# Kernel tuning notes

Measured on AMD Instinct MI355X. Metric: run time of the kernel, lower is better.

Reference implementation:

```python
import jax, jax.numpy as jnp
import numpy as np

B, GS, IN, HID = 256, 32, 512, 1024
HW = GS * GS

def setup_inputs() -> dict:
    key = jax.random.key(0)
    ks = jax.random.split(key, 18)
    s = 0.02
    return {
        "grid": jax.random.normal(ks[0], (B, 1, GS, GS), jnp.float32),
        "conv1_w": jax.random.normal(ks[1], (8, 1, 3, 3), jnp.float32) * s,
        "conv1_b": jax.random.normal(ks[2], (8,), jnp.float32) * s,
        "conv2_w": jax.random.normal(ks[3], (16, 8, 3, 3), jnp.float32) * s,
        "conv2_b": jax.random.normal(ks[4], (16,), jnp.float32) * s,
        "lin_w": jax.random.normal(ks[5], (IN, HW * 16), jnp.float32) * s,
        "lin_b": jax.random.normal(ks[6], (IN,), jnp.float32) * s,
        "gru_wih": jax.random.normal(ks[7], (3 * HID, IN + HW + 1), jnp.float32) * s,
        "gru_whh": jax.random.normal(ks[8], (3 * HID, HID), jnp.float32) * s,
        "gru_bih": jax.random.normal(ks[9], (3 * HID,), jnp.float32) * s,
        "gru_bhh": jax.random.normal(ks[10], (3 * HID,), jnp.float32) * s,
        "write_w": jax.random.normal(ks[11], (HW, HID), jnp.float32) * s,
        "write_b": jax.random.normal(ks[12], (HW,), jnp.float32) * s,
        "inc_w": jax.random.normal(ks[13], (1, HID), jnp.float32) * s,
        "inc_b": jax.random.normal(ks[14], (1,), jnp.float32) * s,
        "term_w": jax.random.normal(ks[15], (1, HID), jnp.float32) * s,
        "term_b": jax.random.normal(ks[16], (1,), jnp.float32) * s,
        "max_steps": 100,
    }

def _conv(x, w, b):
    y = jax.lax.conv_general_dilated(x, w, (1, 1), "SAME",
                                     dimension_numbers=("NCHW", "OIHW", "NCHW"))
    return y + b[None, :, None, None]

def _gru_cell(x, h, wih, whh, bih, bhh):
    gi = x @ wih.T + bih            # (B, 3H)
    gh = h @ whh.T + bhh
    ir, iz, inn = jnp.split(gi, 3, axis=1)
    hr, hz, hn = jnp.split(gh, 3, axis=1)
    r = jax.nn.sigmoid(ir + hr)
    z = jax.nn.sigmoid(iz + hz)
    n = jnp.tanh(inn + r * hn)
    return (1.0 - z) * n + z * h

def reference(grid, conv1_w, conv1_b, conv2_w, conv2_b, lin_w, lin_b,
              gru_wih, gru_whh, gru_bih, gru_bhh,
              write_w, write_b, inc_w, inc_b, term_w, term_b, max_steps):
    bsz = grid.shape[0]
    feat = jax.nn.relu(_conv(grid, conv1_w, conv1_b))
    feat = jax.nn.relu(_conv(feat, conv2_w, conv2_b))
    feat = feat.reshape(bsz, -1) @ lin_w.T + lin_b     # (B, IN), torch Flatten is channel-major

    def step(carry, _):
        h, mask, count, done = carry
        x = jnp.concatenate([feat, mask, count], axis=1)
        h2 = _gru_cell(x, h, gru_wih, gru_whh, gru_bih, gru_bhh)
        write = jax.nn.sigmoid(h2 @ write_w.T + write_b)
        inc = jax.nn.sigmoid(h2 @ inc_w.T + inc_b)
        term = jax.nn.sigmoid(h2 @ term_w.T + term_b)
        upd = jnp.logical_not(done)
        h_n = jnp.where(upd, h2, h)
        mask_n = jnp.where(upd, mask + write, mask)
        count_n = jnp.where(upd, count + inc, count)
        done_n = jnp.logical_or(done, jnp.all(term > 0.5))
        return (h_n, mask_n, count_n, done_n), None

    init = (jnp.zeros((bsz, HID), grid.dtype),
            jnp.zeros((bsz, HW), grid.dtype),
            jnp.zeros((bsz, 1), grid.dtype),
            jnp.array(False))
    (h, mask, count, done), _ = jax.lax.scan(step, init, None, length=max_steps)
    return count, mask
```

## Files before the change

kernel.cpp:

```cpp
#include <hip/hip_runtime.h>
#include <hip/hip_bf16.h>
#include <hip/hip_cooperative_groups.h>

namespace cg = cooperative_groups;

#define DEVI static __device__ __forceinline__

typedef __attribute__((ext_vector_type(8))) short s8v;
typedef __attribute__((ext_vector_type(4))) float f32x4;
typedef unsigned short us_t;
typedef unsigned int u32;

constexpr int NT_ = 256;
constexpr int B_ = 256, HW_ = 1024, IN_ = 512, HID_ = 1024, H3_ = 3072;
constexpr int XD_ = 1537;
constexpr int FLAT_ = 16384;

constexpr int OFF_WIHFBF = 0;
constexpr int OFF_WIHM2  = 393216;
constexpr int OFF_WIHC   = 5111808;
constexpr int OFF_CNTD   = 5114880;
constexpr int OFF_FLAGS  = 5115136;
constexpr int OFF_FEATBF = 5115264;
constexpr int OFF_GI     = 5180800;
constexpr int OFF_GH     = 5967232;
constexpr int OFF_H0     = 6753664;
constexpr int OFF_H1     = 7015808;
constexpr int OFF_WSIG   = 7277952;
constexpr int OFF_HHI    = 7540096;
constexpr int OFF_WSIG2  = 7671168;
constexpr int OFF_C2BF   = 7933312;
constexpr int OFF_PART = OFF_GI;
constexpr int OFF_PW   = OFF_C2BF;
constexpr int OFF_PA2  = 14224768;

struct Params {
  const float* grid;
  const float* c1w; const float* c1b;
  const float* c2w; const float* c2b;
  const float* linw; const float* linb;
  const float* wih; const float* whh;
  const float* bih; const float* bhh;
  const float* ww;  const float* wb;
  const float* incw; const float* incb;
  const float* termw; const float* termb;
  const int* max_steps;
  float* out;
  float* ws;
};

DEVI float sigm(float x) { return 1.f / (1.f + __expf(-x)); }
DEVI float tanh_(float x) { return 1.f - 2.f / (__expf(2.f * x) + 1.f); }
DEVI float2 ld2(const float* p) { return *(const float2*)p; }
DEVI void ld4(float* d, const float* p) {
  float4 v = *(const float4*)p; d[0] = v.x; d[1] = v.y; d[2] = v.z; d[3] = v.w;
}
DEVI us_t f2bf(float x) {
  union { float f; u32 u; } v; v.f = x;
  u32 r = v.u + 0x7FFFu + ((v.u >> 16) & 1u);
  return (us_t)(r >> 16);
}
DEVI float bf2f(us_t h) {
  union { u32 u; float f; } v; v.u = ((u32)h) << 16; return v.f;
}
DEVI u32 pack2(float a, float b) { return (u32)f2bf(a) | ((u32)f2bf(b) << 16); }
DEVI u32 pack2c(float a, float b) {
  __hip_bfloat162 h = __float22bfloat162_rn(make_float2(a, b));
  union { __hip_bfloat162 h; u32 u; } v; v.h = h; return v.u;
}

DEVI s8v ld8w(const us_t* p) { return *(const s8v*)p; }
DEVI s8v ld8w(const float* p) {
  float4 v0 = *(const float4*)p;
  float4 v1 = *(const float4*)(p + 4);
  union { u32 u[4]; s8v s; } r;
  r.u[0] = pack2c(v0.x, v0.y); r.u[1] = pack2c(v0.z, v0.w);
  r.u[2] = pack2c(v1.x, v1.y); r.u[3] = pack2c(v1.z, v1.w);
  return r.s;
}

__global__ __launch_bounds__(NT_) void conv_kernel(Params p) {
  __shared__ float s_in[34 * 34];
  __shared__ float s_c1[8 * 34 * 34];
  const int b = blockIdx.x;
  const int tid = threadIdx.x;
  for (int i = tid; i < 34 * 34; i += NT_) s_in[i] = 0.f;
  for (int i = tid; i < 8 * 34 * 34; i += NT_) s_c1[i] = 0.f;
  __syncthreads();
  for (int i = tid; i < 1024; i += NT_) {
    int y = i >> 5, x = i & 31;
    s_in[(y + 1) * 34 + (x + 1)] = p.grid[b * 1024 + i];
  }
  __syncthreads();
  const int pos0 = tid * 4;
  const int y = pos0 >> 5, x0 = pos0 & 31;
  {
    float win[3][6];
    #pragma unroll
    for (int dy = 0; dy < 3; ++dy)
      #pragma unroll
      for (int c = 0; c < 6; ++c) win[dy][c] = s_in[(y + dy) * 34 + x0 + c];
    float acc[8][4];
    #pragma unroll
    for (int oc = 0; oc < 8; ++oc)
      #pragma unroll
      for (int i = 0; i < 4; ++i) acc[oc][i] = p.c1b[oc];
    #pragma unroll
    for (int oc = 0; oc < 8; ++oc)
      #pragma unroll
      for (int dy = 0; dy < 3; ++dy)
        #pragma unroll
        for (int dx = 0; dx < 3; ++dx) {
          float w = p.c1w[oc * 9 + dy * 3 + dx];
          #pragma unroll
          for (int i = 0; i < 4; ++i)
            acc[oc][i] = fmaf(w, win[dy][i + dx], acc[oc][i]);
        }
    #pragma unroll
    for (int oc = 0; oc < 8; ++oc)
      #pragma unroll
      for (int i = 0; i < 4; ++i)
        s_c1[oc * 1156 + (y + 1) * 34 + (x0 + i + 1)] = fmaxf(acc[oc][i], 0.f);
  }
  __syncthreads();
  {
    float acc[16][4];
    #pragma unroll
    for (int oc = 0; oc < 16; ++oc)
      #pragma unroll
      for (int i = 0; i < 4; ++i) acc[oc][i] = p.c2b[oc];
    for (int ic = 0; ic < 8; ++ic) {
      float win[3][6];
      #pragma unroll
      for (int dy = 0; dy < 3; ++dy)
        #pragma unroll
        for (int c = 0; c < 6; ++c)
          win[dy][c] = s_c1[ic * 1156 + (y + dy) * 34 + x0 + c];
      #pragma unroll
      for (int oc = 0; oc < 16; ++oc)
        #pragma unroll
        for (int dy = 0; dy < 3; ++dy)
          #pragma unroll
          for (int dx = 0; dx < 3; ++dx) {
            float w = p.c2w[oc * 72 + ic * 9 + dy * 3 + dx];
            #pragma unroll
            for (int i = 0; i < 4; ++i)
              acc[oc][i] = fmaf(w, win[dy][i + dx], acc[oc][i]);
          }
    }
    us_t* dst = (us_t*)(p.ws + OFF_C2BF) + b * FLAT_;
    #pragma unroll
    for (int oc = 0; oc < 16; ++oc) {
      u32 lo = pack2(fmaxf(acc[oc][0], 0.f), fmaxf(acc[oc][1], 0.f));
      u32 hi = pack2(fmaxf(acc[oc][2], 0.f), fmaxf(acc[oc][3], 0.f));
      *(uint2*)(dst + oc * 1024 + pos0) = make_uint2(lo, hi);
    }
  }
}

template <typename TA, typename TB>
DEVI void mfma_blockT(const TA* __restrict__ Ag, int lda,
                      const TB* __restrict__ Bg, int ldb, int nc,
                      us_t* __restrict__ sA, us_t* __restrict__ sB,
                      float* __restrict__ dst, int ldd) {
  const int tid = threadIdx.x;
  const int ar = tid >> 3, au = tid & 7;
  const int sw = au ^ (ar & 7);
  const int abase = (ar * 8 + sw) * 8;
  const TA* a0p = Ag + (size_t)ar * lda + au * 8;
  const TA* a1p = Ag + (size_t)(ar + 32) * lda + au * 8;
  const TB* b0p = Bg + (size_t)ar * ldb + au * 8;
  const TB* b1p = b0p + (size_t)32 * ldb;
  const TB* b2p = b0p + (size_t)64 * ldb;
  const TB* b3p = b0p + (size_t)96 * ldb;
  f32x4 acc[4][2];
  #pragma unroll
  for (int f = 0; f < 4; ++f) { acc[f][0] = (f32x4)0.f; acc[f][1] = (f32x4)0.f; }
  s8v ra0 = ld8w(a0p);
  s8v ra1 = ld8w(a1p);
  s8v rb0 = ld8w(b0p);
  s8v rb1 = ld8w(b1p);
  s8v rb2 = ld8w(b2p);
  s8v rb3 = ld8w(b3p);
  const int w = tid >> 6;
  const int lane = tid & 63;
  const int l15 = lane & 15, l4 = lane >> 4;
  const int rsw = l15 & 7;
  int c = 0;
  for (;;) {
    __syncthreads();
    *(s8v*)(sA + abase) = ra0;
    *(s8v*)(sA + abase + 2048) = ra1;
    *(s8v*)(sB + abase) = rb0;
    *(s8v*)(sB + abase + 2048) = rb1;
    *(s8v*)(sB + abase + 4096) = rb2;
    *(s8v*)(sB + abase + 6144) = rb3;
    ++c;
    if (c < nc) {
      const int ko = c * 64;
      ra0 = ld8w(a0p + ko);
      ra1 = ld8w(a1p + ko);
      rb0 = ld8w(b0p + ko);
      rb1 = ld8w(b1p + ko);
      rb2 = ld8w(b2p + ko);
      rb3 = ld8w(b3p + ko);
    }
    __syncthreads();
    #pragma unroll
    for (int kk = 0; kk < 2; ++kk) {
      const int uoff = ((kk * 4 + l4) ^ rsw) * 8;
      s8v bA = *(const s8v*)(sB + (w * 32 + l15) * 64 + uoff);
      s8v bB = *(const s8v*)(sB + (w * 32 + 16 + l15) * 64 + uoff);
      #pragma unroll
      for (int f = 0; f < 4; ++f) {
        s8v a = *(const s8v*)(sA + (f * 16 + l15) * 64 + uoff);
        acc[f][0] = __builtin_amdgcn_mfma_f32_16x16x32_bf16(a, bA, acc[f][0], 0, 0, 0);
        acc[f][1] = __builtin_amdgcn_mfma_f32_16x16x32_bf16(a, bB, acc[f][1], 0, 0, 0);
      }
    }
    if (c >= nc) break;
  }
  #pragma unroll
  for (int f = 0; f < 4; ++f)
    #pragma unroll
    for (int g = 0; g < 2; ++g) {
      float* dp = dst + (size_t)(f * 16 + l4 * 4) * ldd + w * 32 + g * 16 + l15;
      #pragma unroll
      for (int j = 0; j < 4; ++j) dp[(size_t)j * ldd] = acc[f][g][j];
    }
}

__global__ __launch_bounds__(NT_) void lin_mfma(Params p) {
  __shared__ us_t sm[12288];
  const int j = (blockIdx.x >> 3) + (blockIdx.x & 7) * 32;
  const int mt = j & 3, nt = (j >> 2) & 3, ks = j >> 4;
  const us_t* A = (us_t*)(p.ws + OFF_C2BF) + (size_t)mt * 64 * FLAT_ + ks * 1024;
  const float* B = p.linw + (size_t)nt * 128 * FLAT_ + ks * 1024;
  float* dst = p.ws + OFF_PART + ks * (B_ * IN_) + mt * 64 * IN_ + nt * 128;
  mfma_blockT(A, FLAT_, B, FLAT_, 16, sm, sm + 4096, dst, IN_);
}

__global__ __launch_bounds__(NT_) void prepred_kernel(Params p) {
  const int tid = threadIdx.x;
  if (blockIdx.x < 512) {
    const int gt = blockIdx.x * NT_ + tid;
    const int o = gt & (IN_ - 1);
    const float* part = p.ws + OFF_PART;
    float s = p.linb[o];
    #pragma unroll
    for (int ks = 0; ks < 16; ++ks) s += part[ks * (B_ * IN_) + gt];
    ((us_t*)(p.ws + OFF_FEATBF))[gt] = f2bf(s);
  } else {
    const int gt = (blockIdx.x - 512) * NT_ + tid;
    const int gs = 1024 * NT_;
    us_t* wihf = (us_t*)(p.ws + OFF_WIHFBF);
    us_t* wihm2 = (us_t*)(p.ws + OFF_WIHM2);
    float* wihc = p.ws + OFF_WIHC;
    int* flags = (int*)(p.ws + OFF_FLAGS);
    for (int i = gt; i < H3_ * XD_; i += gs) {
      const int n = i / XD_, k = i - n * XD_;
      const float v = p.wih[i];
      if (k < 512) {
        wihf[n * 512 + k] = f2bf(v);
      } else if (k < 1536) {
        const int kk = k - 512;
        const us_t hi = f2bf(v);
        wihm2[n * 2048 + kk] = hi;
        wihm2[n * 2048 + 1024 + kk] = f2bf(v - bf2f(hi));
      } else {
        wihc[n] = v;
      }
    }
    if (gt < 128) flags[gt] = 1;
  }
}

__global__ __launch_bounds__(NT_) void a1_mfma(Params p) {
  __shared__ us_t sm[12288];
  const int b = blockIdx.x;
  const int mt = b / 24, nt = b - mt * 24;
  const us_t* A = (us_t*)(p.ws + OFF_FEATBF) + (size_t)mt * 64 * IN_;
  const us_t* B = (us_t*)(p.ws + OFF_WIHFBF) + (size_t)nt * 128 * IN_;
  float* dst = p.ws + OFF_GI + (size_t)mt * 64 * H3_ + nt * 128;
  mfma_blockT(A, IN_, B, IN_, 8, sm, sm + 4096, dst, H3_);
}

__global__ __launch_bounds__(NT_) void stepA_mfma(Params p, int step) {
  if (((volatile int*)(p.ws + OFF_FLAGS))[step - 1]) return;
  __shared__ us_t sm[12288];
  const int b = blockIdx.x;
  if (b < 576) {
    const int term = b / 192;
    const int r = b - term * 192;
    const int ks = r / 96;
    const int t = r - ks * 96;
    const int mt = t / 24, nt = t - mt * 24;
    const us_t* A = (us_t*)(p.ws + OFF_WSIG2) + (size_t)mt * 64 * 2048 +
                    (term == 1 ? 1024 : 0) + ks * 512;
    const us_t* B = (us_t*)(p.ws + OFF_WIHM2) + (size_t)nt * 128 * 2048 +
                    (term == 2 ? 1024 : 0) + ks * 512;
    float* dst = p.ws + OFF_PA2 + (size_t)(term * 2 + ks) * 786432 +
                 (size_t)mt * 64 * H3_ + nt * 128;
    mfma_blockT(A, 2048, B, 2048, 8, sm, sm + 4096, dst, H3_);
  } else {
    const int r = b - 576;
    const int ks = r / 96;
    const int t = r - ks * 96;
    const int mt = t / 24, nt = t - mt * 24;
    const us_t* A = (us_t*)(p.ws + OFF_HHI) + (size_t)mt * 64 * HID_ + ks * 512;
    const float* B = p.whh + (size_t)nt * 128 * HID_ + ks * 512;
    float* dst = p.ws + OFF_PA2 + (size_t)(6 + ks) * 786432 +
                 (size_t)mt * 64 * H3_ + nt * 128;
    mfma_blockT(A, HID_, B, HID_, 8, sm, sm + 4096, dst, H3_);
  }
}

__global__ __launch_bounds__(NT_) void stepG_kernel(Params p, int step) {
  int* flags = (int*)(p.ws + OFF_FLAGS);
  if (step > 0 && ((volatile int*)flags)[step - 1]) return;
  __shared__ float sred[8];
  const int row = blockIdx.x;
  const int tid = threadIdx.x;
  const size_t base = (size_t)row * H3_;
  float* const gi = p.ws + OFF_GI + base;
  const float* const pA = p.ws + OFF_PA2;
  const float* const wihc = p.ws + OFF_WIHC;
  const float* hold = p.ws + ((step & 1) ? OFF_H1 : OFF_H0) + (size_t)row * HID_;
  float* hnew = p.ws + ((step & 1) ? OFF_H0 : OFF_H1) + (size_t)row * HID_;
  us_t* hhi = (us_t*)(p.ws + OFF_HHI) + (size_t)row * HID_;
  const float cd = (step > 0) ? (p.ws + OFF_CNTD)[row] : 0.f;
  float incd = 0.f, termd = 0.f;
  #pragma unroll
  for (int q = 0; q < 4; ++q) {
    const int c = tid + q * NT_;
    float gr_ = gi[c], gz_ = gi[1024 + c], gn_ = gi[2048 + c];
    float hr_ = 0.f, hz_ = 0.f, hn_ = 0.f, hv = 0.f;
    if (step > 0) {
      #pragma unroll
      for (int t6 = 0; t6 < 6; ++t6) {
        const float* pp = pA + (size_t)t6 * 786432 + base;
        gr_ += pp[c]; gz_ += pp[1024 + c]; gn_ += pp[2048 + c];
      }
      gr_ += cd * wihc[c];
      gz_ += cd * wihc[1024 + c];
      gn_ += cd * wihc[2048 + c];
      const float* q6 = pA + (size_t)6 * 786432 + base;
      const float* q7 = pA + (size_t)7 * 786432 + base;
      hr_ = q6[c] + q7[c];
      hz_ = q6[1024 + c] + q7[1024 + c];
      hn_ = q6[2048 + c] + q7[2048 + c];
      gi[c] = gr_; gi[1024 + c] = gz_; gi[2048 + c] = gn_;
      hv = hold[c];
    }
    float rr = sigm(gr_ + p.bih[c] + hr_ + p.bhh[c]);
    float zz = sigm(gz_ + p.bih[1024 + c] + hz_ + p.bhh[1024 + c]);
    float nn = tanh_(gn_ + p.bih[2048 + c] + rr * (hn_ + p.bhh[2048 + c]));
    float h2 = (1.f - zz) * nn + zz * hv;
    hnew[c] = h2;
    hhi[c] = f2bf(h2);
    incd = fmaf(h2, p.incw[c], incd);
    termd = fmaf(h2, p.termw[c], termd);
  }
  #pragma unroll
  for (int off = 32; off > 0; off >>= 1) {
    incd += __shfl_down(incd, off);
    termd += __shfl_down(termd, off);
  }
  if ((tid & 63) == 0) { sred[tid >> 6] = incd; sred[4 + (tid >> 6)] = termd; }
  __syncthreads();
  if (tid == 0) {
    float it = sred[0] + sred[1] + sred[2] + sred[3];
    float tt = sred[4] + sred[5] + sred[6] + sred[7];
    float cdn = sigm(it + p.incb[0]);
    (p.ws + OFF_CNTD)[row] = cdn;
    if (step == 0) p.out[row] = cdn;
    else p.out[row] += cdn;
    if (tt + p.termb[0] <= 0.f) atomicAnd(&flags[step], 0);
  }
}

__global__ __launch_bounds__(NT_) void stepW_mfma(Params p, int step) {
  if (step > 0 && ((volatile int*)(p.ws + OFF_FLAGS))[step - 1]) return;
  __shared__ us_t sm[12288];
  const int b = blockIdx.x;
  const int ks = b & 7, t = b >> 3;
  const int mt = t >> 3, nt = t & 7;
  const us_t* A = (us_t*)(p.ws + OFF_HHI) + (size_t)mt * 64 * HID_ + ks * 128;
  const float* B = p.ww + (size_t)nt * 128 * HID_ + ks * 128;
  float* dst = p.ws + OFF_PW + ks * (B_ * HW_) + (size_t)mt * 64 * HW_ + nt * 128;
  mfma_blockT(A, HID_, B, HID_, 2, sm, sm + 4096, dst, HW_);
}

__global__ __launch_bounds__(NT_) void stepWepi_kernel(Params p, int step) {
  if (step > 0 && ((volatile int*)(p.ws + OFF_FLAGS))[step - 1]) return;
  const int i = (blockIdx.x * NT_ + threadIdx.x) * 4;
  const int m = i >> 10, n = i & 1023;
  const float* pW = p.ws + OFF_PW;
  float4 s = *(const float4*)(p.wb + n);
  #pragma unroll
  for (int ks = 0; ks < 8; ++ks) {
    float4 v = *(const float4*)(pW + ks * (B_ * HW_) + i);
    s.x += v.x; s.y += v.y; s.z += v.z; s.w += v.w;
  }
  float4 sv = {sigm(s.x), sigm(s.y), sigm(s.z), sigm(s.w)};
  float* op = p.out + B_ + i;
  if (step == 0) {
    *(float4*)op = sv;
  } else {
    float4 ov = *(float4*)op;
    ov.x += sv.x; ov.y += sv.y; ov.z += sv.z; ov.w += sv.w;
    *(float4*)op = ov;
  }
  *(float4*)(p.ws + OFF_WSIG + i) = sv;
  us_t* w2 = (us_t*)(p.ws + OFF_WSIG2) + (size_t)m * 2048 + n;
  us_t h0 = f2bf(sv.x), h1 = f2bf(sv.y), h2b = f2bf(sv.z), h3 = f2bf(sv.w);
  *(uint2*)w2 = make_uint2((u32)h0 | ((u32)h1 << 16), (u32)h2b | ((u32)h3 << 16));
  *(uint2*)(w2 + 1024) = make_uint2(
      pack2(sv.x - bf2f(h0), sv.y - bf2f(h1)),
      pack2(sv.z - bf2f(h2b), sv.w - bf2f(h3)));
}

DEVI void b_job(const Params& p, float* sh2, float* swb,
                const float* gi, const float* gh, const float* hold,
                float* hnew, float* wsig, float* cntd, int* dflag, int job) {
  const int tid = threadIdx.x;
  const int mt = job >> 3, nt = job & 7;
  const int r0 = mt * 8, c0 = nt * 128;
  const int gr = tid >> 5;
  const int gk = (tid & 31) * 2;
  const int wr = tid & 7;
  const int wc = (tid >> 3) * 4;
  const int row = r0 + gr;
  const float* giR = gi + row * H3_;
  const float* ghR = gh + row * H3_;
  const float* hR = hold + row * HID_;
  float* hW = hnew + row * HID_;
  float acc[4] = {0.f, 0.f, 0.f, 0.f};
  float incd = 0.f, termd = 0.f;
  const bool wh = (nt == 0);
  for (int kc = 0; kc < HID_; kc += 64) {
    float2 gxr = ld2(giR + kc + gk);
    float2 gxz = ld2(giR + 1024 + kc + gk);
    float2 gxn = ld2(giR + 2048 + kc + gk);
    float2 ghr = ld2(ghR + kc + gk);
    float2 ghz = ld2(ghR + 1024 + kc + gk);
    float2 ghn = ld2(ghR + 2048 + kc + gk);
    float2 hol = ld2(hR + kc + gk);
    float2 bri = ld2(p.bih + kc + gk);
    float2 brh = ld2(p.bhh + kc + gk);
    float2 bzi = ld2(p.bih + 1024 + kc + gk);
    float2 bzh = ld2(p.bhh + 1024 + kc + gk);
    float2 bni = ld2(p.bih + 2048 + kc + gk);
    float2 bnh = ld2(p.bhh + 2048 + kc + gk);
    float2 iw = ld2(p.incw + kc + gk);
    float2 tw = ld2(p.termw + kc + gk);
    float h2[2];
    {
      float rr = sigm(gxr.x + bri.x + ghr.x + brh.x);
      float zz = sigm(gxz.x + bzi.x + ghz.x + bzh.x);
      float nn = tanh_(gxn.x + bni.x + rr * (ghn.x + bnh.x));
      h2[0] = (1.f - zz) * nn + zz * hol.x;
      rr = sigm(gxr.y + bri.y + ghr.y + brh.y);
      zz = sigm(gxz.y + bzi.y + ghz.y + bzh.y);
      nn = tanh_(gxn.y + bni.y + rr * (ghn.y + bnh.y));
      h2[1] = (1.f - zz) * nn + zz * hol.y;
    }
    incd = fmaf(h2[0], iw.x, fmaf(h2[1], iw.y, incd));
    termd = fmaf(h2[0], tw.x, fmaf(h2[1], tw.y, termd));
    float4 wreg[8];
    #pragma unroll
    for (int it = 0; it < 8; ++it) {
      int id = tid + it * 256;
      int c = id >> 4, k4 = (id & 15) * 4;
      wreg[it] = *(const float4*)(p.ww + (c0 + c) * HID_ + kc + k4);
    }
    __syncthreads();
    sh2[gr * 68 + gk] = h2[0];
    sh2[gr * 68 + gk + 1] = h2[1];
    #pragma unroll
    for (int it = 0; it < 8; ++it) {
      int id = tid + it * 256;
      int c = id >> 4, k4 = (id & 15) * 4;
      swb[(k4 + 0) * 132 + c] = wreg[it].x;
      swb[(k4 + 1) * 132 + c] = wreg[it].y;
      swb[(k4 + 2) * 132 + c] = wreg[it].z;
      swb[(k4 + 3) * 132 + c] = wreg[it].w;
    }
    if (wh) {
      *(float2*)(hW + kc + gk) = make_float2(h2[0], h2[1]);
      *(u32*)((us_t*)(p.ws + OFF_HHI) + row * HID_ + kc + gk) = pack2(h2[0], h2[1]);
    }
    __syncthreads();
    #pragma unroll 8
    for (int kk = 0; kk < 64; ++kk) {
      float a = sh2[wr * 68 + kk];
      float4 b = *(const float4*)(swb + kk * 132 + wc);
      acc[0] = fmaf(a, b.x, acc[0]);
      acc[1] = fmaf(a, b.y, acc[1]);
      acc[2] = fmaf(a, b.z, acc[2]);
      acc[3] = fmaf(a, b.w, acc[3]);
    }
  }
  if (wh) {
    #pragma unroll
    for (int off = 16; off > 0; off >>= 1) {
      incd += __shfl_down(incd, off, 32);
      termd += __shfl_down(termd, off, 32);
    }
    if ((tid & 31) == 0) {
      float cd = sigm(incd + p.incb[0]);
      cntd[row] = cd;
      p.out[row] += cd;
      if (termd + p.termb[0] <= 0.f) atomicAnd(dflag, 0);
    }
  }
  {
    const int m = r0 + wr;
    float4 wb4 = *(const float4*)(p.wb + c0 + wc);
    float4 sv = {sigm(acc[0] + wb4.x), sigm(acc[1] + wb4.y),
                 sigm(acc[2] + wb4.z), sigm(acc[3] + wb4.w)};
    float* op = p.out + B_ + m * HW_ + c0 + wc;
    float4 ov = *(float4*)op;
    ov.x += sv.x; ov.y += sv.y; ov.z += sv.z; ov.w += sv.w;
    *(float4*)op = ov;
    *(float4*)(wsig + m * HID_ + c0 + wc) = sv;
    us_t* w2 = (us_t*)(p.ws + OFF_WSIG2) + m * 2048 + c0 + wc;
    us_t h0 = f2bf(sv.x), h1 = f2bf(sv.y), h2b = f2bf(sv.z), h3 = f2bf(sv.w);
    *(uint2*)w2 = make_uint2((u32)h0 | ((u32)h1 << 16), (u32)h2b | ((u32)h3 << 16));
    *(uint2*)(w2 + 1024) = make_uint2(
        pack2(sv.x - bf2f(h0), sv.y - bf2f(h1)),
        pack2(sv.z - bf2f(h2b), sv.w - bf2f(h3)));
  }
}

template <bool SB>
DEVI void gemm_db64(const float* __restrict__ A, int lda,
                    const float* __restrict__ Bw, int ldb, int K,
                    float* __restrict__ As, float* __restrict__ Bs,
                    float (&acc)[4][4]) {
  constexpr int P = 68;
  const int tid = threadIdx.x;
  const int tx = tid & 15, ty = tid >> 4;
  const int lr = tid >> 2, lk = (tid & 3) << 2;
  #pragma unroll
  for (int i = 0; i < 4; ++i)
    #pragma unroll
    for (int j = 0; j < 4; ++j) acc[i][j] = 0.f;
  auto ldb4 = [&](int k0) {
    float4 v;
    if constexpr (SB) {
      const float* q = Bw + (size_t)lr * ldb + k0 + lk;
      v.x = q[0]; v.y = q[1]; v.z = q[2]; v.w = q[3];
    } else {
      v = *(const float4*)(Bw + (size_t)lr * ldb + k0 + lk);
    }
    return v;
  };
  float4 va = *(const float4*)(A + lr * lda + lk);
  float4 vb = ldb4(0);
  As[(lk + 0) * P + lr] = va.x; As[(lk + 1) * P + lr] = va.y;
  As[(lk + 2) * P + lr] = va.z; As[(lk + 3) * P + lr] = va.w;
  Bs[(lk + 0) * P + lr] = vb.x; Bs[(lk + 1) * P + lr] = vb.y;
  Bs[(lk + 2) * P + lr] = vb.z; Bs[(lk + 3) * P + lr] = vb.w;
  __syncthreads();
  int cur = 0;
  for (int k0 = 16; k0 < K; k0 += 16) {
    va = *(const float4*)(A + lr * lda + k0 + lk);
    vb = ldb4(k0);
    const float* as = As + cur * (16 * P);
    const float* bs = Bs + cur * (16 * P);
    #pragma unroll
    for (int kk = 0; kk < 16; ++kk) {
      float a[4], b[4];
      ld4(a, as + kk * P + ty * 4);
      ld4(b, bs + kk * P + tx * 4);
      #pragma unroll
      for (int i = 0; i < 4; ++i)
        #pragma unroll
        for (int j = 0; j < 4; ++j) acc[i][j] = fmaf(a[i], b[j], acc[i][j]);
    }
    __syncthreads();
    float* asw = As + (cur ^ 1) * (16 * P);
    float* bsw = Bs + (cur ^ 1) * (16 * P);
    asw[(lk + 0) * P + lr] = va.x; asw[(lk + 1) * P + lr] = va.y;
    asw[(lk + 2) * P + lr] = va.z; asw[(lk + 3) * P + lr] = va.w;
    bsw[(lk + 0) * P + lr] = vb.x; bsw[(lk + 1) * P + lr] = vb.y;
    bsw[(lk + 2) * P + lr] = vb.z; bsw[(lk + 3) * P + lr] = vb.w;
    __syncthreads();
    cur ^= 1;
  }
  const float* as = As + cur * (16 * P);
  const float* bs = Bs + cur * (16 * P);
  #pragma unroll
  for (int kk = 0; kk < 16; ++kk) {
    float a[4], b[4];
    ld4(a, as + kk * P + ty * 4);
    ld4(b, bs + kk * P + tx * 4);
    #pragma unroll
    for (int i = 0; i < 4; ++i)
      #pragma unroll
      for (int j = 0; j < 4; ++j) acc[i][j] = fmaf(a[i], b[j], acc[i][j]);
  }
}

__global__ __launch_bounds__(NT_, 2) void tail_kernel(Params p, int start) {
  int* flags = (int*)(p.ws + OFF_FLAGS);
  if (((volatile int*)flags)[start - 1]) return;
  cg::grid_group gg = cg::this_grid();
  __shared__ __align__(16) float smem[8992];
  float* As = smem;
  float* Bs = smem + 2176;
  float* sh2 = smem;
  float* swb = smem + 544;
  float* const ws = p.ws;
  float* const gi = ws + OFF_GI;
  float* const gh = ws + OFF_GH;
  float* const wsig = ws + OFF_WSIG;
  float* const cntd = ws + OFF_CNTD;
  const float* const wihc = ws + OFF_WIHC;
  const int tid = threadIdx.x;
  const int bid = blockIdx.x;
  const int nb = gridDim.x;
  const int tx = tid & 15, ty = tid >> 4;
  const int msteps = p.max_steps[0];

  for (int step = start; step < msteps; ++step) {
    float* hcur = ws + ((step & 1) ? OFF_H1 : OFF_H0);
    float* hnxt = ws + ((step & 1) ? OFF_H0 : OFF_H1);
    for (int job = bid; job < 384; job += nb) {
      float acc[4][4];
      if (job < 192) {
        const int mt = job / 48, nt = job - mt * 48;
        gemm_db64<true>(wsig + mt * 64 * HID_, HID_,
                        p.wih + (size_t)nt * 64 * XD_ + 512, XD_, HID_, As, Bs, acc);
        #pragma unroll
        for (int i = 0; i < 4; ++i) {
          const int m = mt * 64 + ty * 4 + i;
          const float cd = cntd[m];
          float4 wc4 = *(const float4*)(wihc + nt * 64 + tx * 4);
          float* gp = gi + m * H3_ + nt * 64 + tx * 4;
          float4 g = *(float4*)gp;
          g.x += acc[i][0] + cd * wc4.x;
          g.y += acc[i][1] + cd * wc4.y;
          g.z += acc[i][2] + cd * wc4.z;
          g.w += acc[i][3] + cd * wc4.w;
          *(float4*)gp = g;
        }
      } else {
        const int j = job - 192;
        const int mt = j / 48, nt = j - mt * 48;
        gemm_db64<false>(hcur + mt * 64 * HID_, HID_,
                         p.whh + (size_t)nt * 64 * HID_, HID_, HID_, As, Bs, acc);
        #pragma unroll
        for (int i = 0; i < 4; ++i) {
          float4 v = {acc[i][0], acc[i][1], acc[i][2], acc[i][3]};
          *(float4*)(gh + (mt * 64 + ty * 4 + i) * H3_ + nt * 64 + tx * 4) = v;
        }
      }
      __syncthreads();
    }
    gg.sync();
    for (int job = bid; job < 256; job += nb)
      b_job(p, sh2, swb, gi, gh, hcur, hnxt, wsig, cntd, &flags[step], job);
    gg.sync();
    if (((volatile int*)flags)[step]) break;
  }
}

extern "C" void kernel_launch(void* const* d_in, const int* in_sizes, int n_in,
                              void* d_out, int out_size, void* d_ws, size_t ws_size,
                              hipStream_t stream) {
  (void)in_sizes; (void)n_in; (void)out_size; (void)ws_size;
  Params prm;
  prm.grid = (const float*)d_in[0];
  prm.c1w  = (const float*)d_in[1];
  prm.c1b  = (const float*)d_in[2];
  prm.c2w  = (const float*)d_in[3];
  prm.c2b  = (const float*)d_in[4];
  prm.linw = (const float*)d_in[5];
  prm.linb = (const float*)d_in[6];
  prm.wih  = (const float*)d_in[7];
  prm.whh  = (const float*)d_in[8];
  prm.bih  = (const float*)d_in[9];
  prm.bhh  = (const float*)d_in[10];
  prm.ww   = (const float*)d_in[11];
  prm.wb   = (const float*)d_in[12];
  prm.incw = (const float*)d_in[13];
  prm.incb = (const float*)d_in[14];
  prm.termw = (const float*)d_in[15];
  prm.termb = (const float*)d_in[16];
  prm.max_steps = (const int*)d_in[17];
  prm.out = (float*)d_out;
  prm.ws = (float*)d_ws;

  hipLaunchKernelGGL(conv_kernel, dim3(B_), dim3(NT_), 0, stream, prm);
  hipLaunchKernelGGL(lin_mfma, dim3(256), dim3(NT_), 0, stream, prm);
  hipLaunchKernelGGL(prepred_kernel, dim3(1536), dim3(NT_), 0, stream, prm);
  hipLaunchKernelGGL(a1_mfma, dim3(96), dim3(NT_), 0, stream, prm);

  constexpr int U = 2;
  hipLaunchKernelGGL(stepG_kernel, dim3(B_), dim3(NT_), 0, stream, prm, 0);
  hipLaunchKernelGGL(stepW_mfma, dim3(256), dim3(NT_), 0, stream, prm, 0);
  hipLaunchKernelGGL(stepWepi_kernel, dim3(256), dim3(NT_), 0, stream, prm, 0);
  for (int t = 1; t < U; ++t) {
    hipLaunchKernelGGL(stepA_mfma, dim3(768), dim3(NT_), 0, stream, prm, t);
    hipLaunchKernelGGL(stepG_kernel, dim3(B_), dim3(NT_), 0, stream, prm, t);
    hipLaunchKernelGGL(stepW_mfma, dim3(256), dim3(NT_), 0, stream, prm, t);
    hipLaunchKernelGGL(stepWepi_kernel, dim3(256), dim3(NT_), 0, stream, prm, t);
  }
  int start = U;
  void* args[] = {(void*)&prm, (void*)&start};
  (void)hipLaunchCooperativeKernel((const void*)tail_kernel, dim3(384), dim3(NT_),
                                   args, 0, stream);
}
```

Measured before the change: 142.8 us.

## Drop Wih preconversion pass; convert weights on the fly and fuse step GEMMs

Removes the prepass that converted gru_wih into bf16 hi/lo workspace copies. The weights are now read as fp32 directly from the original matrix inside the MFMA loaders, with the hi/lo split computed on load. The step-1 Wih and Whh GEMMs are restructured into K-unsplit 32-row tiles that accumulate straight into gi and gh, removing the eight partial buffers and their reduction in stepG. The Whh GEMM for step 1 is folded into the step-0 stepW launch, and the flag init moves into conv_kernel. This trades a one-time conversion pass and extra memory traffic for repeated per-call fp32 loads with conversion arithmetic, and strided column reads of the count weight.

```diff
diff --git a/kernel.cpp b/kernel.cpp
--- a/kernel.cpp
+++ b/kernel.cpp
@@ -16,9 +16,6 @@
 constexpr int XD_ = 1537;
 constexpr int FLAT_ = 16384;
 
-constexpr int OFF_WIHFBF = 0;
-constexpr int OFF_WIHM2  = 393216;
-constexpr int OFF_WIHC   = 5111808;
 constexpr int OFF_CNTD   = 5114880;
 constexpr int OFF_FLAGS  = 5115136;
 constexpr int OFF_FEATBF = 5115264;
@@ -32,7 +29,6 @@
 constexpr int OFF_C2BF   = 7933312;
 constexpr int OFF_PART = OFF_GI;
 constexpr int OFF_PW   = OFF_C2BF;
-constexpr int OFF_PA2  = 14224768;
 
 struct Params {
   const float* grid;
@@ -64,18 +60,27 @@
   union { u32 u; float f; } v; v.u = ((u32)h) << 16; return v.f;
 }
 DEVI u32 pack2(float a, float b) { return (u32)f2bf(a) | ((u32)f2bf(b) << 16); }
-DEVI u32 pack2c(float a, float b) {
-  __hip_bfloat162 h = __float22bfloat162_rn(make_float2(a, b));
-  union { __hip_bfloat162 h; u32 u; } v; v.h = h; return v.u;
-}
 
 DEVI s8v ld8w(const us_t* p) { return *(const s8v*)p; }
 DEVI s8v ld8w(const float* p) {
   float4 v0 = *(const float4*)p;
   float4 v1 = *(const float4*)(p + 4);
   union { u32 u[4]; s8v s; } r;
-  r.u[0] = pack2c(v0.x, v0.y); r.u[1] = pack2c(v0.z, v0.w);
-  r.u[2] = pack2c(v1.x, v1.y); r.u[3] = pack2c(v1.z, v1.w);
+  r.u[0] = pack2(v0.x, v0.y); r.u[1] = pack2(v0.z, v0.w);
+  r.u[2] = pack2(v1.x, v1.y); r.u[3] = pack2(v1.z, v1.w);
+  return r.s;
+}
+struct wihu { const float* p; int lo; };
+DEVI wihu operator+(wihu a, size_t d) { return {a.p + d, a.lo}; }
+DEVI wihu operator+(wihu a, int d) { return {a.p + d, a.lo}; }
+DEVI s8v ld8w(wihu a) {
+  union { u32 u[4]; s8v s; } r;
+  #pragma unroll
+  for (int i = 0; i < 4; ++i) {
+    float x = a.p[2 * i], y = a.p[2 * i + 1];
+    if (a.lo) { x = x - bf2f(f2bf(x)); y = y - bf2f(f2bf(y)); }
+    r.u[i] = pack2(x, y);
+  }
   return r.s;
 }
 
@@ -84,6 +89,7 @@
   __shared__ float s_c1[8 * 34 * 34];
   const int b = blockIdx.x;
   const int tid = threadIdx.x;
+  if (b == 0 && tid < 128) ((int*)(p.ws + OFF_FLAGS))[tid] = 1;
   for (int i = tid; i < 34 * 34; i += NT_) s_in[i] = 0.f;
   for (int i = tid; i < 8 * 34 * 34; i += NT_) s_c1[i] = 0.f;
   __syncthreads();
@@ -158,21 +164,20 @@
   }
 }
 
-template <typename TA, typename TB>
-DEVI void mfma_blockT(const TA* __restrict__ Ag, int lda,
-                      const TB* __restrict__ Bg, int ldb, int nc,
+template <typename AA, typename BA>
+DEVI void mfma_blockT(AA Ag, int lda, BA Bg, int ldb, int nc,
                       us_t* __restrict__ sA, us_t* __restrict__ sB,
                       float* __restrict__ dst, int ldd) {
   const int tid = threadIdx.x;
   const int ar = tid >> 3, au = tid & 7;
   const int sw = au ^ (ar & 7);
   const int abase = (ar * 8 + sw) * 8;
-  const TA* a0p = Ag + (size_t)ar * lda + au * 8;
-  const TA* a1p = Ag + (size_t)(ar + 32) * lda + au * 8;
-  const TB* b0p = Bg + (size_t)ar * ldb + au * 8;
-  const TB* b1p = b0p + (size_t)32 * ldb;
-  const TB* b2p = b0p + (size_t)64 * ldb;
-  const TB* b3p = b0p + (size_t)96 * ldb;
+  auto a0p = Ag + ((size_t)ar * lda + au * 8);
+  auto a1p = Ag + ((size_t)(ar + 32) * lda + au * 8);
+  auto b0p = Bg + ((size_t)ar * ldb + au * 8);
+  auto b1p = Bg + ((size_t)(ar + 32) * ldb + au * 8);
+  auto b2p = Bg + ((size_t)(ar + 64) * ldb + au * 8);
+  auto b3p = Bg + ((size_t)(ar + 96) * ldb + au * 8);
   f32x4 acc[4][2];
   #pragma unroll
   for (int f = 0; f < 4; ++f) { acc[f][0] = (f32x4)0.f; acc[f][1] = (f32x4)0.f; }
@@ -230,6 +235,68 @@
     }
 }
 
+template <typename BA, int NP>
+DEVI void mfma32(const us_t* const (&Ap)[NP], int lda,
+                 const BA (&Bp)[NP], int ldb, int nc,
+                 us_t* __restrict__ sA, us_t* __restrict__ sB,
+                 f32x4 (&acc)[2][2]) {
+  const int tid = threadIdx.x;
+  const int ar = tid >> 3, au = tid & 7;
+  const int sw = au ^ (ar & 7);
+  const int abase = (ar * 8 + sw) * 8;
+  const int w = tid >> 6;
+  const int lane = tid & 63;
+  const int l15 = lane & 15, l4 = lane >> 4;
+  const int rsw = l15 & 7;
+  acc[0][0] = (f32x4)0.f; acc[0][1] = (f32x4)0.f;
+  acc[1][0] = (f32x4)0.f; acc[1][1] = (f32x4)0.f;
+  #pragma unroll
+  for (int pp = 0; pp < NP; ++pp) {
+    const us_t* a0p = Ap[pp] + (size_t)ar * lda + au * 8;
+    auto b0p = Bp[pp] + ((size_t)ar * ldb + au * 8);
+    auto b1p = Bp[pp] + ((size_t)(ar + 32) * ldb + au * 8);
+    auto b2p = Bp[pp] + ((size_t)(ar + 64) * ldb + au * 8);
+    auto b3p = Bp[pp] + ((size_t)(ar + 96) * ldb + au * 8);
+    s8v ra0 = ld8w(a0p);
+    s8v rb0 = ld8w(b0p);
+    s8v rb1 = ld8w(b1p);
+    s8v rb2 = ld8w(b2p);
+    s8v rb3 = ld8w(b3p);
+    int c = 0;
+    for (;;) {
+      __syncthreads();
+      *(s8v*)(sA + abase) = ra0;
+      *(s8v*)(sB + abase) = rb0;
+      *(s8v*)(sB + abase + 2048) = rb1;
+      *(s8v*)(sB + abase + 4096) = rb2;
+      *(s8v*)(sB + abase + 6144) = rb3;
+      ++c;
+      if (c < nc) {
+        const int ko = c * 64;
+        ra0 = ld8w(a0p + ko);
+        rb0 = ld8w(b0p + ko);
+        rb1 = ld8w(b1p + ko);
+        rb2 = ld8w(b2p + ko);
+        rb3 = ld8w(b3p + ko);
+      }
+      __syncthreads();
+      #pragma unroll
+      for (int kk = 0; kk < 2; ++kk) {
+        const int uoff = ((kk * 4 + l4) ^ rsw) * 8;
+        s8v bA = *(const s8v*)(sB + (w * 32 + l15) * 64 + uoff);
+        s8v bB = *(const s8v*)(sB + (w * 32 + 16 + l15) * 64 + uoff);
+        #pragma unroll
+        for (int f = 0; f < 2; ++f) {
+          s8v a = *(const s8v*)(sA + (f * 16 + l15) * 64 + uoff);
+          acc[f][0] = __builtin_amdgcn_mfma_f32_16x16x32_bf16(a, bA, acc[f][0], 0, 0, 0);
+          acc[f][1] = __builtin_amdgcn_mfma_f32_16x16x32_bf16(a, bB, acc[f][1], 0, 0, 0);
+        }
+      }
+      if (c >= nc) break;
+    }
+  }
+}
+
 __global__ __launch_bounds__(NT_) void lin_mfma(Params p) {
   __shared__ us_t sm[12288];
   const int j = (blockIdx.x >> 3) + (blockIdx.x & 7) * 32;
@@ -240,39 +307,14 @@
   mfma_blockT(A, FLAT_, B, FLAT_, 16, sm, sm + 4096, dst, IN_);
 }
 
-__global__ __launch_bounds__(NT_) void prepred_kernel(Params p) {
-  const int tid = threadIdx.x;
-  if (blockIdx.x < 512) {
-    const int gt = blockIdx.x * NT_ + tid;
-    const int o = gt & (IN_ - 1);
-    const float* part = p.ws + OFF_PART;
-    float s = p.linb[o];
-    #pragma unroll
-    for (int ks = 0; ks < 16; ++ks) s += part[ks * (B_ * IN_) + gt];
-    ((us_t*)(p.ws + OFF_FEATBF))[gt] = f2bf(s);
-  } else {
-    const int gt = (blockIdx.x - 512) * NT_ + tid;
-    const int gs = 1024 * NT_;
-    us_t* wihf = (us_t*)(p.ws + OFF_WIHFBF);
-    us_t* wihm2 = (us_t*)(p.ws + OFF_WIHM2);
-    float* wihc = p.ws + OFF_WIHC;
-    int* flags = (int*)(p.ws + OFF_FLAGS);
-    for (int i = gt; i < H3_ * XD_; i += gs) {
-      const int n = i / XD_, k = i - n * XD_;
-      const float v = p.wih[i];
-      if (k < 512) {
-        wihf[n * 512 + k] = f2bf(v);
-      } else if (k < 1536) {
-        const int kk = k - 512;
-        const us_t hi = f2bf(v);
-        wihm2[n * 2048 + kk] = hi;
-        wihm2[n * 2048 + 1024 + kk] = f2bf(v - bf2f(hi));
-      } else {
-        wihc[n] = v;
-      }
-    }
-    if (gt < 128) flags[gt] = 1;
-  }
+__global__ __launch_bounds__(NT_) void red_kernel(Params p) {
+  const int gt = blockIdx.x * NT_ + threadIdx.x;
+  const int o = gt & (IN_ - 1);
+  const float* part = p.ws + OFF_PART;
+  float s = p.linb[o];
+  #pragma unroll
+  for (int ks = 0; ks < 16; ++ks) s += part[ks * (B_ * IN_) + gt];
+  ((us_t*)(p.ws + OFF_FEATBF))[gt] = f2bf(s);
 }
 
 __global__ __launch_bounds__(NT_) void a1_mfma(Params p) {
@@ -280,39 +322,39 @@
   const int b = blockIdx.x;
   const int mt = b / 24, nt = b - mt * 24;
   const us_t* A = (us_t*)(p.ws + OFF_FEATBF) + (size_t)mt * 64 * IN_;
-  const us_t* B = (us_t*)(p.ws + OFF_WIHFBF) + (size_t)nt * 128 * IN_;
+  wihu B = {p.wih + (size_t)(nt * 128) * XD_, 0};
   float* dst = p.ws + OFF_GI + (size_t)mt * 64 * H3_ + nt * 128;
-  mfma_blockT(A, IN_, B, IN_, 8, sm, sm + 4096, dst, H3_);
+  mfma_blockT(A, IN_, B, XD_, 8, sm, sm + 4096, dst, H3_);
 }
 
 __global__ __launch_bounds__(NT_) void stepA_mfma(Params p, int step) {
   if (((volatile int*)(p.ws + OFF_FLAGS))[step - 1]) return;
-  __shared__ us_t sm[12288];
-  const int b = blockIdx.x;
-  if (b < 576) {
-    const int term = b / 192;
-    const int r = b - term * 192;
-    const int ks = r / 96;
-    const int t = r - ks * 96;
-    const int mt = t / 24, nt = t - mt * 24;
-    const us_t* A = (us_t*)(p.ws + OFF_WSIG2) + (size_t)mt * 64 * 2048 +
-                    (term == 1 ? 1024 : 0) + ks * 512;
-    const us_t* B = (us_t*)(p.ws + OFF_WIHM2) + (size_t)nt * 128 * 2048 +
-                    (term == 2 ? 1024 : 0) + ks * 512;
-    float* dst = p.ws + OFF_PA2 + (size_t)(term * 2 + ks) * 786432 +
-                 (size_t)mt * 64 * H3_ + nt * 128;
-    mfma_blockT(A, 2048, B, 2048, 8, sm, sm + 4096, dst, H3_);
-  } else {
-    const int r = b - 576;
-    const int ks = r / 96;
-    const int t = r - ks * 96;
-    const int mt = t / 24, nt = t - mt * 24;
-    const us_t* A = (us_t*)(p.ws + OFF_HHI) + (size_t)mt * 64 * HID_ + ks * 512;
-    const float* B = p.whh + (size_t)nt * 128 * HID_ + ks * 512;
-    float* dst = p.ws + OFF_PA2 + (size_t)(6 + ks) * 786432 +
-                 (size_t)mt * 64 * H3_ + nt * 128;
-    mfma_blockT(A, HID_, B, HID_, 8, sm, sm + 4096, dst, H3_);
-  }
+  __shared__ us_t sm[10240];
+  const int r = blockIdx.x;
+  const int j = (r >> 3) + (r & 7) * 24;
+  const int mt = j & 7, nt = j >> 3;
+  const us_t* ws2 = (us_t*)(p.ws + OFF_WSIG2) + (size_t)mt * 32 * 2048;
+  const float* wb = p.wih + (size_t)(nt * 128) * XD_ + 512;
+  const us_t* Ap[3] = {ws2, ws2 + 1024, ws2};
+  const wihu Bp[3] = {{wb, 0}, {wb, 0}, {wb, 1}};
+  f32x4 acc[2][2];
+  mfma32(Ap, 2048, Bp, XD_, 16, sm, sm + 2048, acc);
+  const int w = threadIdx.x >> 6, lane = threadIdx.x & 63;
+  const int l15 = lane & 15, l4 = lane >> 4;
+  float* const gi = p.ws + OFF_GI;
+  const float* const cntd = p.ws + OFF_CNTD;
+  #pragma unroll
+  for (int f = 0; f < 2; ++f)
+    #pragma unroll
+    for (int g = 0; g < 2; ++g) {
+      const int col = nt * 128 + w * 32 + g * 16 + l15;
+      const float wc = p.wih[(size_t)col * XD_ + 1536];
+      #pragma unroll
+      for (int jj = 0; jj < 4; ++jj) {
+        const int row = mt * 32 + f * 16 + l4 * 4 + jj;
+        gi[(size_t)row * H3_ + col] += acc[f][g][jj] + cntd[row] * wc;
+      }
+    }
 }
 
 __global__ __launch_bounds__(NT_) void stepG_kernel(Params p, int step) {
@@ -322,13 +364,11 @@
   const int row = blockIdx.x;
   const int tid = threadIdx.x;
   const size_t base = (size_t)row * H3_;
-  float* const gi = p.ws + OFF_GI + base;
-  const float* const pA = p.ws + OFF_PA2;
-  const float* const wihc = p.ws + OFF_WIHC;
+  const float* const gi = p.ws + OFF_GI + base;
+  const float* const gh = p.ws + OFF_GH + base;
   const float* hold = p.ws + ((step & 1) ? OFF_H1 : OFF_H0) + (size_t)row * HID_;
   float* hnew = p.ws + ((step & 1) ? OFF_H0 : OFF_H1) + (size_t)row * HID_;
   us_t* hhi = (us_t*)(p.ws + OFF_HHI) + (size_t)row * HID_;
-  const float cd = (step > 0) ? (p.ws + OFF_CNTD)[row] : 0.f;
   float incd = 0.f, termd = 0.f;
   #pragma unroll
   for (int q = 0; q < 4; ++q) {
@@ -336,20 +376,7 @@
     float gr_ = gi[c], gz_ = gi[1024 + c], gn_ = gi[2048 + c];
     float hr_ = 0.f, hz_ = 0.f, hn_ = 0.f, hv = 0.f;
     if (step > 0) {
-      #pragma unroll
-      for (int t6 = 0; t6 < 6; ++t6) {
-        const float* pp = pA + (size_t)t6 * 786432 + base;
-        gr_ += pp[c]; gz_ += pp[1024 + c]; gn_ += pp[2048 + c];
-      }
-      gr_ += cd * wihc[c];
-      gz_ += cd * wihc[1024 + c];
-      gn_ += cd * wihc[2048 + c];
-      const float* q6 = pA + (size_t)6 * 786432 + base;
-      const float* q7 = pA + (size_t)7 * 786432 + base;
-      hr_ = q6[c] + q7[c];
-      hz_ = q6[1024 + c] + q7[1024 + c];
-      hn_ = q6[2048 + c] + q7[2048 + c];
-      gi[c] = gr_; gi[1024 + c] = gz_; gi[2048 + c] = gn_;
+      hr_ = gh[c]; hz_ = gh[1024 + c]; hn_ = gh[2048 + c];
       hv = hold[c];
     }
     float rr = sigm(gr_ + p.bih[c] + hr_ + p.bhh[c]);
@@ -380,15 +407,41 @@
 }
 
 __global__ __launch_bounds__(NT_) void stepW_mfma(Params p, int step) {
-  if (step > 0 && ((volatile int*)(p.ws + OFF_FLAGS))[step - 1]) return;
   __shared__ us_t sm[12288];
   const int b = blockIdx.x;
-  const int ks = b & 7, t = b >> 3;
-  const int mt = t >> 3, nt = t & 7;
-  const us_t* A = (us_t*)(p.ws + OFF_HHI) + (size_t)mt * 64 * HID_ + ks * 128;
-  const float* B = p.ww + (size_t)nt * 128 * HID_ + ks * 128;
-  float* dst = p.ws + OFF_PW + ks * (B_ * HW_) + (size_t)mt * 64 * HW_ + nt * 128;
-  mfma_blockT(A, HID_, B, HID_, 2, sm, sm + 4096, dst, HW_);
+  int* flags = (int*)(p.ws + OFF_FLAGS);
+  if (b < 256) {
+    if (step > 0 && ((volatile int*)flags)[step - 1]) return;
+    const int ks = b & 7, t = b >> 3;
+    const int mt = t >> 3, nt = t & 7;
+    const us_t* A = (us_t*)(p.ws + OFF_HHI) + (size_t)mt * 64 * HID_ + ks * 128;
+    const float* B = p.ww + (size_t)nt * 128 * HID_ + ks * 128;
+    float* dst = p.ws + OFF_PW + ks * (B_ * HW_) + (size_t)mt * 64 * HW_ + nt * 128;
+    mfma_blockT(A, HID_, B, HID_, 2, sm, sm + 4096, dst, HW_);
+  } else {
+    if (((volatile int*)flags)[step]) return;
+    const int r = b - 256;
+    const int j = (r >> 3) + (r & 7) * 24;
+    const int mt = j & 7, nt = j >> 3;
+    const us_t* Ap[1] = {(us_t*)(p.ws + OFF_HHI) + (size_t)mt * 32 * HID_};
+    const float* Bp[1] = {p.whh + (size_t)(nt * 128) * HID_};
+    f32x4 acc[2][2];
+    mfma32(Ap, HID_, Bp, HID_, 16, sm, sm + 2048, acc);
+    const int w = threadIdx.x >> 6, lane = threadIdx.x & 63;
+    const int l15 = lane & 15, l4 = lane >> 4;
+    float* const gh = p.ws + OFF_GH;
+    #pragma unroll
+    for (int f = 0; f < 2; ++f)
+      #pragma unroll
+      for (int g = 0; g < 2; ++g) {
+        const int col = nt * 128 + w * 32 + g * 16 + l15;
+        #pragma unroll
+        for (int jj = 0; jj < 4; ++jj) {
+          const int row = mt * 32 + f * 16 + l4 * 4 + jj;
+          gh[(size_t)row * H3_ + col] = acc[f][g][jj];
+        }
+      }
+  }
 }
 
 __global__ __launch_bounds__(NT_) void stepWepi_kernel(Params p, int step) {
@@ -617,7 +670,6 @@
   float* const gh = ws + OFF_GH;
   float* const wsig = ws + OFF_WSIG;
   float* const cntd = ws + OFF_CNTD;
-  const float* const wihc = ws + OFF_WIHC;
   const int tid = threadIdx.x;
   const int bid = blockIdx.x;
   const int nb = gridDim.x;
@@ -637,13 +689,16 @@
         for (int i = 0; i < 4; ++i) {
           const int m = mt * 64 + ty * 4 + i;
           const float cd = cntd[m];
-          float4 wc4 = *(const float4*)(wihc + nt * 64 + tx * 4);
+          float wc4[4];
+          #pragma unroll
+          for (int q = 0; q < 4; ++q)
+            wc4[q] = p.wih[(size_t)(nt * 64 + tx * 4 + q) * XD_ + 1536];
           float* gp = gi + m * H3_ + nt * 64 + tx * 4;
           float4 g = *(float4*)gp;
-          g.x += acc[i][0] + cd * wc4.x;
-          g.y += acc[i][1] + cd * wc4.y;
-          g.z += acc[i][2] + cd * wc4.z;
-          g.w += acc[i][3] + cd * wc4.w;
+          g.x += acc[i][0] + cd * wc4[0];
+          g.y += acc[i][1] + cd * wc4[1];
+          g.z += acc[i][2] + cd * wc4[2];
+          g.w += acc[i][3] + cd * wc4[3];
           *(float4*)gp = g;
         }
       } else {
@@ -695,20 +750,18 @@
 
   hipLaunchKernelGGL(conv_kernel, dim3(B_), dim3(NT_), 0, stream, prm);
   hipLaunchKernelGGL(lin_mfma, dim3(256), dim3(NT_), 0, stream, prm);
-  hipLaunchKernelGGL(prepred_kernel, dim3(1536), dim3(NT_), 0, stream, prm);
+  hipLaunchKernelGGL(red_kernel, dim3(512), dim3(NT_), 0, stream, prm);
   hipLaunchKernelGGL(a1_mfma, dim3(96), dim3(NT_), 0, stream, prm);
 
-  constexpr int U = 2;
   hipLaunchKernelGGL(stepG_kernel, dim3(B_), dim3(NT_), 0, stream, prm, 0);
-  hipLaunchKernelGGL(stepW_mfma, dim3(256), dim3(NT_), 0, stream, prm, 0);
+  hipLaunchKernelGGL(stepW_mfma, dim3(448), dim3(NT_), 0, stream, prm, 0);
   hipLaunchKernelGGL(stepWepi_kernel, dim3(256), dim3(NT_), 0, stream, prm, 0);
-  for (int t = 1; t < U; ++t) {
-    hipLaunchKernelGGL(stepA_mfma, dim3(768), dim3(NT_), 0, stream, prm, t);
-    hipLaunchKernelGGL(stepG_kernel, dim3(B_), dim3(NT_), 0, stream, prm, t);
-    hipLaunchKernelGGL(stepW_mfma, dim3(256), dim3(NT_), 0, stream, prm, t);
-    hipLaunchKernelGGL(stepWepi_kernel, dim3(256), dim3(NT_), 0, stream, prm, t);
-  }
-  int start = U;
+  hipLaunchKernelGGL(stepA_mfma, dim3(192), dim3(NT_), 0, stream, prm, 1);
+  hipLaunchKernelGGL(stepG_kernel, dim3(B_), dim3(NT_), 0, stream, prm, 1);
+  hipLaunchKernelGGL(stepW_mfma, dim3(256), dim3(NT_), 0, stream, prm, 1);
+  hipLaunchKernelGGL(stepWepi_kernel, dim3(256), dim3(NT_), 0, stream, prm, 1);
+
+  int start = 2;
   void* args[] = {(void*)&prm, (void*)&start};
   (void)hipLaunchCooperativeKernel((const void*)tail_kernel, dim3(384), dim3(NT_),
                                    args, 0, stream);
```

New measurement: 188.2 us. 31.9% more time.
